# Kernel optimization log

Hardware: AMD Instinct MI355X
Metric: run time of the kernel (lower is better)

The kernel has to match this reference:

```python
import jax, jax.numpy as jnp
import numpy as np

B, S, E, H = 2, 2048, 2048, 32
D = E // H  # head_dim = 64
SCALE = D ** -0.5


def setup_inputs() -> dict:
    key = jax.random.key(0)
    ks = jax.random.split(key, 9)
    std = E ** -0.5
    return {
        "hidden_states": jax.random.normal(ks[0], (B, S, E), dtype=jnp.float32),
        "Wq": jax.random.normal(ks[1], (E, E), dtype=jnp.float32) * std,
        "bq": jax.random.normal(ks[2], (E,), dtype=jnp.float32) * 0.02,
        "Wk": jax.random.normal(ks[3], (E, E), dtype=jnp.float32) * std,
        "bk": jax.random.normal(ks[4], (E,), dtype=jnp.float32) * 0.02,
        "Wv": jax.random.normal(ks[5], (E, E), dtype=jnp.float32) * std,
        "bv": jax.random.normal(ks[6], (E,), dtype=jnp.float32) * 0.02,
        "Wo": jax.random.normal(ks[7], (E, E), dtype=jnp.float32) * std,
        "bo": jax.random.normal(ks[8], (E,), dtype=jnp.float32) * 0.02,
    }


def reference(hidden_states, Wq, bq, Wk, bk, Wv, bv, Wo, bo):
    # QKV projections (torch Linear: x @ W.T + b)
    q = hidden_states @ Wq.T + bq  # [B,S,E]
    k = hidden_states @ Wk.T + bk
    v = hidden_states @ Wv.T + bv
    # split heads -> [B,S,H,D]
    q = q.reshape(B, S, H, D)
    k = k.reshape(B, S, H, D)
    v = v.reshape(B, S, H, D)
    # causal scaled dot-product attention (prefill path of paged attention)
    scores = jnp.einsum("bqhd,bkhd->bhqk", q, k) * SCALE  # [B,H,S,S]
    causal = jnp.tril(jnp.ones((S, S), dtype=bool))
    scores = jnp.where(causal, scores, jnp.finfo(scores.dtype).min)
    probs = jax.nn.softmax(scores, axis=-1)
    attn = jnp.einsum("bhqk,bkhd->bqhd", probs, v).reshape(B, S, E)
    # output projection
    return attn @ Wo.T + bo
```

## Files before the change

kernel.cpp:

```cpp
#include <hip/hip_runtime.h>
#include <hip/hip_bf16.h>

#define B_ 2
#define S_ 2048
#define E_ 2048
#define H_ 32
#define D_ 64
#define SCALE_L2E 0.18033688f

typedef __attribute__((ext_vector_type(8))) short short8_t;
typedef __attribute__((ext_vector_type(4))) float float4_t;
typedef __attribute__((ext_vector_type(16))) float f32x16;
typedef unsigned int uint;
typedef __attribute__((ext_vector_type(4))) uint uint4_t;

__device__ __forceinline__ short f2bf(float f) {
  union { float f; unsigned u; } x; x.f = f;
  unsigned r = x.u + 0x7fffu + ((x.u >> 16) & 1u);
  return (short)(r >> 16);
}

__device__ __forceinline__ void gload_lds16(const void* g, void* l) {
  __builtin_amdgcn_global_load_lds((const __attribute__((address_space(1))) void*)g,
                                   (__attribute__((address_space(3))) void*)l, 16, 0, 0);
}

__device__ __forceinline__ uint cvt_pk_bf16(float lo, float hi) {
  uint r;
  asm volatile("v_cvt_pk_bf16_f32 %0, %1, %2" : "=v"(r) : "v"(lo), "v"(hi));
  return r;
}

__device__ __forceinline__ void pl32swap(uint& a, uint& b) {
  asm volatile("v_permlane32_swap_b32 %0, %1" : "+v"(a), "+v"(b));
}

__device__ __forceinline__ f32x16 zero16() {
  f32x16 v;
#pragma unroll
  for (int i = 0; i < 16; ++i) v[i] = 0.f;
  return v;
}

__global__ void cast_bf16_kernel(const float* __restrict__ in, short* __restrict__ out, int n4) {
  const int stride = gridDim.x * blockDim.x;
  for (int j = blockIdx.x * blockDim.x + threadIdx.x; j < n4; j += stride) {
    const float4 v = ((const float4*)in)[j];
    short4 r;
    r.x = f2bf(v.x); r.y = f2bf(v.y); r.z = f2bf(v.z); r.w = f2bf(v.w);
    ((short4*)out)[j] = r;
  }
}

__global__ void cast3_bf16(const float* __restrict__ a, const float* __restrict__ b,
                           const float* __restrict__ c, short* __restrict__ out) {
  constexpr int n4 = (E_ * E_) / 4;
  const int stride = gridDim.x * blockDim.x;
  for (int j = blockIdx.x * blockDim.x + threadIdx.x; j < 3 * n4; j += stride) {
    const float* src = (j < n4) ? a : (j < 2 * n4 ? b : c);
    const int idx = j & (n4 - 1);
    const float4 v = ((const float4*)src)[idx];
    short4 r;
    r.x = f2bf(v.x); r.y = f2bf(v.y); r.z = f2bf(v.z); r.w = f2bf(v.w);
    ((short4*)out)[j] = r;
  }
}

__global__ __launch_bounds__(512, 2) void gemm384_qkv(const short* __restrict__ A,
                                                      const short* __restrict__ Wt,
                                                      const float* __restrict__ bq,
                                                      const float* __restrict__ bk,
                                                      const float* __restrict__ bv,
                                                      short* __restrict__ Qb,
                                                      short* __restrict__ Kb,
                                                      short* __restrict__ Vb) {
  extern __shared__ __align__(16) char lds[];
  constexpr int K = E_, NT = K / 64;
  const int tid = threadIdx.x, w = tid >> 6, lane = tid & 63;
  const int wr = w >> 2, wc = w & 3;
  const int m0 = blockIdx.y * 128, n0 = blockIdx.x * 384;
  const int l15 = lane & 15, l4 = lane >> 4;

  const int sr = lane >> 2;
  const int ss = lane & 3;
  const char* aBase;
  const char* bBase[3];
  {
    const int ra = w * 16 + sr;
    aBase = (const char*)A + (size_t)(m0 + ra) * (K * 2) + ((ss ^ ((ra >> 1) & 3)) * 16);
#pragma unroll
    for (int g = 0; g < 3; ++g) {
      const int rb = g * 128 + w * 16 + sr;
      bBase[g] = (const char*)Wt + (size_t)(n0 + rb) * (K * 2) + ((ss ^ ((rb >> 1) & 3)) * 16);
    }
  }

  auto stageA = [&](int buf, int ks, int kt) {
    gload_lds16(aBase + kt * 128 + ks * 64, lds + (buf * 2 + ks) * 8192 + w * 1024);
  };
  auto stageB = [&](int buf, int ks, int kt) {
    char* base = lds + 32768 + (buf * 2 + ks) * 24576 + w * 1024;
#pragma unroll
    for (int g = 0; g < 3; ++g)
      gload_lds16(bBase[g] + kt * 128 + ks * 64, base + g * 8192);
  };
  auto ldA = [&](int buf, int ks, int i) {
    const int lr = wr * 64 + i * 16 + l15;
    return *(const short8_t*)(lds + (buf * 2 + ks) * 8192 + lr * 64 +
                              ((l4 * 16) ^ (((lr >> 1) & 3) << 4)));
  };
  auto ldB = [&](int buf, int ks, int j) {
    const int lc = wc * 96 + j * 16 + l15;
    return *(const short8_t*)(lds + 32768 + (buf * 2 + ks) * 24576 + lc * 64 +
                              ((l4 * 16) ^ (((lc >> 1) & 3) << 4)));
  };

  float4_t acc[4][6];
#pragma unroll
  for (int i = 0; i < 4; ++i)
#pragma unroll
    for (int j = 0; j < 6; ++j) acc[i][j] = (float4_t){0.f, 0.f, 0.f, 0.f};

  stageA(0, 0, 0);
  stageB(0, 0, 0);
  stageA(0, 1, 0);
  stageB(0, 1, 0);

  short8_t a_[4], b_[6];
  for (int t = 0; t < NT; ++t) {
    const int c = t & 1;
#pragma unroll
    for (int ks = 0; ks < 2; ++ks) {
      if (t + 1 < NT) {
        stageA(c ^ 1, ks, t + 1);
        stageB(c ^ 1, ks, t + 1);
        asm volatile("s_waitcnt vmcnt(8)" ::: "memory");
      } else if (ks == 0) {
        asm volatile("s_waitcnt vmcnt(4)" ::: "memory");
      } else {
        asm volatile("s_waitcnt vmcnt(0)" ::: "memory");
      }
      __builtin_amdgcn_s_barrier();
      asm volatile("" ::: "memory");
#pragma unroll
      for (int i = 0; i < 4; ++i) a_[i] = ldA(c, ks, i);
#pragma unroll
      for (int j = 0; j < 6; ++j) b_[j] = ldB(c, ks, j);
      asm volatile("s_waitcnt lgkmcnt(0)" ::: "memory");
      __builtin_amdgcn_sched_barrier(0);
      __builtin_amdgcn_s_setprio(1);
#pragma unroll
      for (int i = 0; i < 4; ++i)
#pragma unroll
        for (int j = 0; j < 6; ++j)
          acc[i][j] = __builtin_amdgcn_mfma_f32_16x16x32_bf16(a_[i], b_[j], acc[i][j], 0, 0, 0);
      __builtin_amdgcn_s_setprio(0);
    }
  }

  __syncthreads();
  const int rg = l4 * 4;
  const int b = m0 >> 11;
  const int mloc = m0 & (S_ - 1);
  char* scratch = lds + w * 2048;
#pragma unroll
  for (int j = 0; j < 6; ++j) {
    const int gc0 = n0 + wc * 96 + j * 16;
    const int seg = gc0 >> 11;
    const int ncol = gc0 & 2047;
    if (seg == 2) {
      const float bvv = bv[ncol + l15];
      asm volatile("" ::: "memory");
#pragma unroll
      for (int i = 0; i < 4; ++i) {
        short4 v;
        v.x = f2bf(acc[i][j][0] + bvv);
        v.y = f2bf(acc[i][j][1] + bvv);
        v.z = f2bf(acc[i][j][2] + bvv);
        v.w = f2bf(acc[i][j][3] + bvv);
        *(short4*)(scratch + l15 * 128 + (((i * 16 + rg) * 2) ^ ((l15 & 7) << 4))) = v;
      }
      asm volatile("s_waitcnt lgkmcnt(0)" ::: "memory");
      __builtin_amdgcn_sched_barrier(0);
#pragma unroll
      for (int half = 0; half < 2; ++half) {
        const int n = (lane >> 3) + half * 8;
        const int mb = (lane & 7) * 16;
        const short8_t vv =
            *(const short8_t*)(scratch + n * 128 + (mb ^ ((n & 7) << 4)));
        *(short8_t*)(Vb + ((size_t)(b * E_ + ncol + n)) * S_ + mloc + wr * 64 + (mb >> 1)) = vv;
      }
      asm volatile("s_waitcnt lgkmcnt(0)" ::: "memory");
      __builtin_amdgcn_sched_barrier(0);
    } else {
      const float* bias = seg ? bk : bq;
      short* Out = seg ? Kb : Qb;
      const float sc = seg ? 1.0f : SCALE_L2E;
      const int col = ncol + l15;
      const float bvv = bias[col];
#pragma unroll
      for (int i = 0; i < 4; ++i)
#pragma unroll
        for (int ii = 0; ii < 4; ++ii)
          Out[(size_t)(m0 + wr * 64 + i * 16 + rg + ii) * E_ + col] =
              f2bf((acc[i][j][ii] + bvv) * sc);
    }
  }
}

__global__ __launch_bounds__(512, 2) void gemm_o8(const short* __restrict__ A,
                                                  const short* __restrict__ Wt,
                                                  const float* __restrict__ bias,
                                                  float* __restrict__ Fout) {
  extern __shared__ __align__(16) char lds[];
  constexpr int K = E_, NT = K / 64;
  const int tid = threadIdx.x, w = tid >> 6, lane = tid & 63;
  const int wr = w >> 2, wc = w & 3;
  const int m0 = blockIdx.y * 128, n0 = blockIdx.x * 256;
  const int l15 = lane & 15, l4 = lane >> 4;

  const int sr = lane >> 2;
  const int ss = lane & 3;
  const char* aBase;
  const char* bBase0;
  const char* bBase1;
  {
    const int ra = w * 16 + sr;
    aBase = (const char*)A + (size_t)(m0 + ra) * (K * 2) + ((ss ^ ((ra >> 1) & 3)) * 16);
    const int rb0 = w * 16 + sr;
    bBase0 = (const char*)Wt + (size_t)(n0 + rb0) * (K * 2) + ((ss ^ ((rb0 >> 1) & 3)) * 16);
    const int rb1 = 128 + w * 16 + sr;
    bBase1 = (const char*)Wt + (size_t)(n0 + rb1) * (K * 2) + ((ss ^ ((rb1 >> 1) & 3)) * 16);
  }

  auto stageA = [&](int dbuf, int ks, int kt) {
    gload_lds16(aBase + kt * 128 + ks * 64, lds + (dbuf * 2 + ks) * 8192 + w * 1024);
  };
  auto stageB = [&](int dbuf, int ks, int kt) {
    char* base = lds + 32768 + (dbuf * 2 + ks) * 16384 + w * 1024;
    gload_lds16(bBase0 + kt * 128 + ks * 64, base);
    gload_lds16(bBase1 + kt * 128 + ks * 64, base + 8192);
  };
  auto ldA = [&](int dbuf, int ks, int i) {
    const int lr = wr * 64 + i * 16 + l15;
    return *(const short8_t*)(lds + (dbuf * 2 + ks) * 8192 + lr * 64 +
                              ((l4 * 16) ^ (((lr >> 1) & 3) << 4)));
  };
  auto ldB = [&](int dbuf, int ks, int j) {
    const int lc = wc * 64 + j * 16 + l15;
    return *(const short8_t*)(lds + 32768 + (dbuf * 2 + ks) * 16384 + lc * 64 +
                              ((l4 * 16) ^ (((lc >> 1) & 3) << 4)));
  };

  float4_t acc[4][4];
#pragma unroll
  for (int i = 0; i < 4; ++i)
#pragma unroll
    for (int j = 0; j < 4; ++j) acc[i][j] = (float4_t){0.f, 0.f, 0.f, 0.f};

  stageA(0, 0, 0);
  stageB(0, 0, 0);
  stageA(0, 1, 0);
  stageB(0, 1, 0);

  short8_t a_[4], b_[4];
  for (int t = 0; t < NT; ++t) {
    const int c = t & 1;
#pragma unroll
    for (int ks = 0; ks < 2; ++ks) {
      if (t + 1 < NT) {
        stageA(c ^ 1, ks, t + 1);
        stageB(c ^ 1, ks, t + 1);
        asm volatile("s_waitcnt vmcnt(6)" ::: "memory");
      } else if (ks == 0) {
        asm volatile("s_waitcnt vmcnt(3)" ::: "memory");
      } else {
        asm volatile("s_waitcnt vmcnt(0)" ::: "memory");
      }
      __builtin_amdgcn_s_barrier();
      asm volatile("" ::: "memory");
#pragma unroll
      for (int i = 0; i < 4; ++i) a_[i] = ldA(c, ks, i);
#pragma unroll
      for (int j = 0; j < 4; ++j) b_[j] = ldB(c, ks, j);
      asm volatile("s_waitcnt lgkmcnt(0)" ::: "memory");
      __builtin_amdgcn_sched_barrier(0);
      __builtin_amdgcn_s_setprio(1);
#pragma unroll
      for (int i = 0; i < 4; ++i)
#pragma unroll
        for (int j = 0; j < 4; ++j)
          acc[i][j] = __builtin_amdgcn_mfma_f32_16x16x32_bf16(a_[i], b_[j], acc[i][j], 0, 0, 0);
      __builtin_amdgcn_s_setprio(0);
    }
  }

  const int rg = l4 * 4;
#pragma unroll
  for (int j = 0; j < 4; ++j) {
    const int col = n0 + wc * 64 + j * 16 + l15;
    const float bvv = bias[col];
#pragma unroll
    for (int i = 0; i < 4; ++i)
#pragma unroll
      for (int ii = 0; ii < 4; ++ii)
        Fout[(size_t)(m0 + wr * 64 + i * 16 + rg + ii) * E_ + col] = acc[i][j][ii] + bvv;
  }
}

__global__ __launch_bounds__(512, 2) void attn_fwd(const short* __restrict__ Qg,
                                                   const short* __restrict__ Kg,
                                                   const short* __restrict__ Vt,
                                                   short* __restrict__ Og) {
  __shared__ __align__(16) short lds[16384];
  const int tid = threadIdx.x, w = tid >> 6, lane = tid & 63;
  const int l31 = lane & 31, hh = lane >> 5;
  const int bh = blockIdx.x;
  const int b = bh >> 5, h = bh & 31;
  const int pq = blockIdx.y;

  const char* Kgb = (const char*)(Kg + (size_t)b * S_ * E_ + h * D_);
  const char* Vgb = (const char*)(Vt + (size_t)bh * 64 * S_);

  const int srow = w * 8 + (lane >> 3);
  const int sb = (lane & 7) * 16;
  const int ssw = (srow & 7) << 4;

#pragma unroll 1
  for (int ph = 0; ph < 2; ++ph) {
    const int qt = ph ? (7 - pq) : pq;
    const int q0 = qt * 256;
    const int qwmin = q0 + w * 32;
    const int qg = qwmin + l31;

    const short* qr = Qg + ((size_t)(b * S_ + qg)) * E_ + h * D_;
    short8_t qf[4];
#pragma unroll
    for (int dblk = 0; dblk < 4; ++dblk)
      qf[dblk] = *(const short8_t*)(qr + dblk * 16 + hh * 8);

    f32x16 o0 = zero16(), o1 = zero16();
    float m_run = -1e30f, l_run = 0.f;

    const int nt = 4 * qt + 4;
    const int ntw = (qwmin + 31) / 64 + 1;

    gload_lds16(Kgb + (size_t)srow * 4096 + (sb ^ ssw), lds + w * 512);
    gload_lds16(Vgb + (size_t)srow * 4096 + (sb ^ ssw), lds + 4096 + w * 512);
    __syncthreads();

    int cur = 0;
    for (int t = 0; t < nt; ++t) {
      if (t + 1 < nt) {
        const int k0n = (t + 1) * 64;
        short* kb = lds + (cur ^ 1) * 8192 + w * 512;
        gload_lds16(Kgb + (size_t)(k0n + srow) * 4096 + (sb ^ ssw), kb);
        gload_lds16(Vgb + (size_t)srow * 4096 + (size_t)k0n * 2 + (sb ^ ssw), kb + 4096);
      }

      if (t < ntw) {
        const int k0 = t * 64;
        const char* Kc = (const char*)lds + cur * 16384;
        const char* Vc = Kc + 8192;
        const int xs = (l31 & 7) << 4;

        f32x16 st0 = zero16(), st1 = zero16();
#pragma unroll
        for (int dblk = 0; dblk < 4; ++dblk) {
          const int off = (dblk * 32 + hh * 16) ^ xs;
          const short8_t kf0 = *(const short8_t*)(Kc + l31 * 128 + off);
          const short8_t kf1 = *(const short8_t*)(Kc + (32 + l31) * 128 + off);
          st0 = __builtin_amdgcn_mfma_f32_32x32x16_bf16(kf0, qf[dblk], st0, 0, 0, 0);
          st1 = __builtin_amdgcn_mfma_f32_32x32x16_bf16(kf1, qf[dblk], st1, 0, 0, 0);
        }

        if (k0 + 63 > qwmin) {
#pragma unroll
          for (int r = 0; r < 16; ++r) {
            const int kvr = k0 + ((r & 3) + 8 * (r >> 2) + 4 * hh);
            if (kvr > qg) st0[r] = -1e30f;
            if (kvr + 32 > qg) st1[r] = -1e30f;
          }
        }

        float mv = -1e30f;
#pragma unroll
        for (int r = 0; r < 16; ++r) mv = fmaxf(mv, fmaxf(st0[r], st1[r]));
        mv = fmaxf(mv, __shfl_xor(mv, 32));
        const float mnew = fmaxf(m_run, mv);
        const float alpha = exp2f(m_run - mnew);
        m_run = mnew;
        float sum = 0.f;
#pragma unroll
        for (int r = 0; r < 16; ++r) {
          st0[r] = exp2f(st0[r] - mnew);
          st1[r] = exp2f(st1[r] - mnew);
          sum += st0[r] + st1[r];
        }
        sum += __shfl_xor(sum, 32);
        l_run = l_run * alpha + sum;
        o0 = o0 * alpha;
        o1 = o1 * alpha;

        uint pk_[16];
#pragma unroll
        for (int j = 0; j < 8; ++j) pk_[j] = cvt_pk_bf16(st0[2 * j], st0[2 * j + 1]);
#pragma unroll
        for (int j = 0; j < 8; ++j) pk_[8 + j] = cvt_pk_bf16(st1[2 * j], st1[2 * j + 1]);
        pl32swap(pk_[0], pk_[2]);  pl32swap(pk_[1], pk_[3]);
        pl32swap(pk_[4], pk_[6]);  pl32swap(pk_[5], pk_[7]);
        pl32swap(pk_[8], pk_[10]); pl32swap(pk_[9], pk_[11]);
        pl32swap(pk_[12], pk_[14]); pl32swap(pk_[13], pk_[15]);
        uint4_t paw[4];
#pragma unroll
        for (int f = 0; f < 4; ++f)
          paw[f] = (uint4_t){pk_[4 * f], pk_[4 * f + 1], pk_[4 * f + 2], pk_[4 * f + 3]};

#pragma unroll
        for (int kb = 0; kb < 4; ++kb) {
          const short8_t pa = *(const short8_t*)&paw[kb];
          const int off = (kb * 32 + hh * 16) ^ xs;
          const short8_t vf0 = *(const short8_t*)(Vc + l31 * 128 + off);
          const short8_t vf1 = *(const short8_t*)(Vc + (32 + l31) * 128 + off);
          o0 = __builtin_amdgcn_mfma_f32_32x32x16_bf16(vf0, pa, o0, 0, 0, 0);
          o1 = __builtin_amdgcn_mfma_f32_32x32x16_bf16(vf1, pa, o1, 0, 0, 0);
        }
      }

      __syncthreads();
      cur ^= 1;
    }

    {
      short* ow = lds + w * 2048;
      const float inv = 1.0f / l_run;
#pragma unroll
      for (int r = 0; r < 16; ++r) {
        const int d = (r & 3) + 8 * (r >> 2) + 4 * hh;
        const int x = (l31 & 7) << 4;
        *(short*)((char*)ow + l31 * 128 + ((d * 2) ^ x)) = f2bf(o0[r] * inv);
        *(short*)((char*)ow + l31 * 128 + (((d + 32) * 2) ^ x)) = f2bf(o1[r] * inv);
      }
#pragma unroll
      for (int pz = 0; pz < 4; ++pz) {
        const int qloc = pz * 8 + (lane >> 3);
        const int sbyte = (lane & 7) * 16;
        const short8_t vv = *(const short8_t*)((char*)ow + qloc * 128 + (sbyte ^ ((qloc & 7) << 4)));
        *(short8_t*)(Og + ((size_t)(b * S_ + q0 + w * 32 + qloc)) * E_ + h * 64 + (lane & 7) * 8) = vv;
      }
    }
    __syncthreads();
  }
}

extern "C" void kernel_launch(void* const* d_in, const int* in_sizes, int n_in,
                              void* d_out, int out_size, void* d_ws, size_t ws_size,
                              hipStream_t stream) {
  const float* X  = (const float*)d_in[0];
  const float* Wq = (const float*)d_in[1];
  const float* bq = (const float*)d_in[2];
  const float* Wk = (const float*)d_in[3];
  const float* bk = (const float*)d_in[4];
  const float* Wv = (const float*)d_in[5];
  const float* bv = (const float*)d_in[6];
  const float* Wo = (const float*)d_in[7];
  const float* bo = (const float*)d_in[8];

  const size_t NX = (size_t)B_ * S_ * E_;
  const size_t NW = (size_t)E_ * E_;

  short* ws = (short*)d_ws;
  short* Xb = ws;
  short* Wb = Xb + NX;
  short* Kb = Wb + 3 * NW;
  short* Vb = Kb + NX;
  short* Qb = (short*)d_out;
  short* Ab = Xb;

  (void)hipFuncSetAttribute((const void*)gemm384_qkv,
                            hipFuncAttributeMaxDynamicSharedMemorySize, 131072);
  (void)hipFuncSetAttribute((const void*)gemm_o8,
                            hipFuncAttributeMaxDynamicSharedMemorySize, 98304);

  cast_bf16_kernel<<<2048, 256, 0, stream>>>(X, Xb, (int)(NX / 4));
  cast3_bf16<<<3072, 256, 0, stream>>>(Wq, Wk, Wv, Wb);

  gemm384_qkv<<<dim3(16, 32), 512, 131072, stream>>>(Xb, Wb, bq, bk, bv, Qb, Kb, Vb);

  cast_bf16_kernel<<<1024, 256, 0, stream>>>(Wo, Wb, (int)(NW / 4));

  attn_fwd<<<dim3(B_ * H_, 4), 512, 0, stream>>>(Qb, Kb, Vb, Ab);

  gemm_o8<<<dim3(E_ / 256, B_ * S_ / 128), 512, 98304, stream>>>(Ab, Wb, bo, (float*)d_out);
}
```

Before: 251.2 us.

## Split QKV GEMM into 256x256 Q/K GEMM and separate V GEMM, fuse casts

Replaces the single 128x384-tile QKV projection with a 256x256-tile kernel for Q and K and a separate 128x256-tile kernel for V, which keeps the transposed epilogue. The X and Wq/Wk/Wv casts are merged into one launch. The larger Q/K tile raises arithmetic intensity per LDS byte and removes per-column segment branching in the epilogue. The cost is an extra GEMM launch and a smaller V grid that may leave the GPU underfilled, plus higher register use from the 8x4 accumulators.

```diff
diff --git a/kernel.cpp b/kernel.cpp
--- a/kernel.cpp
+++ b/kernel.cpp
@@ -40,6 +40,29 @@
 #pragma unroll
   for (int i = 0; i < 16; ++i) v[i] = 0.f;
   return v;
+}
+
+__global__ void cast_xw(const float* __restrict__ X, const float* __restrict__ Wq,
+                        const float* __restrict__ Wk, const float* __restrict__ Wv,
+                        short* __restrict__ out) {
+  constexpr int nX = 1 << 21, nW = 1 << 20, total = nX + 3 * nW;
+  const int stride = gridDim.x * blockDim.x;
+  for (int j = blockIdx.x * blockDim.x + threadIdx.x; j < total; j += stride) {
+    const float* src;
+    int idx;
+    if (j < nX) {
+      src = X; idx = j;
+    } else {
+      const int jw = j - nX;
+      const int sel = jw >> 20;
+      idx = jw & (nW - 1);
+      src = sel == 0 ? Wq : (sel == 1 ? Wk : Wv);
+    }
+    const float4 v = ((const float4*)src)[idx];
+    short4 r;
+    r.x = f2bf(v.x); r.y = f2bf(v.y); r.z = f2bf(v.z); r.w = f2bf(v.w);
+    ((short4*)out)[j] = r;
+  }
 }
 
 __global__ void cast_bf16_kernel(const float* __restrict__ in, short* __restrict__ out, int n4) {
@@ -52,81 +75,64 @@
   }
 }
 
-__global__ void cast3_bf16(const float* __restrict__ a, const float* __restrict__ b,
-                           const float* __restrict__ c, short* __restrict__ out) {
-  constexpr int n4 = (E_ * E_) / 4;
-  const int stride = gridDim.x * blockDim.x;
-  for (int j = blockIdx.x * blockDim.x + threadIdx.x; j < 3 * n4; j += stride) {
-    const float* src = (j < n4) ? a : (j < 2 * n4 ? b : c);
-    const int idx = j & (n4 - 1);
-    const float4 v = ((const float4*)src)[idx];
-    short4 r;
-    r.x = f2bf(v.x); r.y = f2bf(v.y); r.z = f2bf(v.z); r.w = f2bf(v.w);
-    ((short4*)out)[j] = r;
-  }
-}
-
-__global__ __launch_bounds__(512, 2) void gemm384_qkv(const short* __restrict__ A,
-                                                      const short* __restrict__ Wt,
-                                                      const float* __restrict__ bq,
-                                                      const float* __restrict__ bk,
-                                                      const float* __restrict__ bv,
-                                                      short* __restrict__ Qb,
-                                                      short* __restrict__ Kb,
-                                                      short* __restrict__ Vb) {
+__global__ __launch_bounds__(512, 2) void gemm256_qk(const short* __restrict__ A,
+                                                     const short* __restrict__ Wt,
+                                                     const float* __restrict__ bq,
+                                                     const float* __restrict__ bk,
+                                                     short* __restrict__ Qb,
+                                                     short* __restrict__ Kb) {
   extern __shared__ __align__(16) char lds[];
   constexpr int K = E_, NT = K / 64;
   const int tid = threadIdx.x, w = tid >> 6, lane = tid & 63;
   const int wr = w >> 2, wc = w & 3;
-  const int m0 = blockIdx.y * 128, n0 = blockIdx.x * 384;
+  const int m0 = blockIdx.y * 256, n0 = blockIdx.x * 256;
   const int l15 = lane & 15, l4 = lane >> 4;
 
   const int sr = lane >> 2;
   const int ss = lane & 3;
-  const char* aBase;
-  const char* bBase[3];
-  {
-    const int ra = w * 16 + sr;
-    aBase = (const char*)A + (size_t)(m0 + ra) * (K * 2) + ((ss ^ ((ra >> 1) & 3)) * 16);
-#pragma unroll
-    for (int g = 0; g < 3; ++g) {
-      const int rb = g * 128 + w * 16 + sr;
-      bBase[g] = (const char*)Wt + (size_t)(n0 + rb) * (K * 2) + ((ss ^ ((rb >> 1) & 3)) * 16);
-    }
+  const char* aB[2];
+  const char* bB[2];
+#pragma unroll
+  for (int g = 0; g < 2; ++g) {
+    const int r = w * 32 + g * 16 + sr;
+    aB[g] = (const char*)A + (size_t)(m0 + r) * (K * 2) + ((ss ^ ((r >> 1) & 3)) * 16);
+    bB[g] = (const char*)Wt + (size_t)(n0 + r) * (K * 2) + ((ss ^ ((r >> 1) & 3)) * 16);
   }
 
   auto stageA = [&](int buf, int ks, int kt) {
-    gload_lds16(aBase + kt * 128 + ks * 64, lds + (buf * 2 + ks) * 8192 + w * 1024);
+#pragma unroll
+    for (int g = 0; g < 2; ++g)
+      gload_lds16(aB[g] + kt * 128 + ks * 64, lds + (buf * 2 + ks) * 16384 + w * 2048 + g * 1024);
   };
   auto stageB = [&](int buf, int ks, int kt) {
-    char* base = lds + 32768 + (buf * 2 + ks) * 24576 + w * 1024;
-#pragma unroll
-    for (int g = 0; g < 3; ++g)
-      gload_lds16(bBase[g] + kt * 128 + ks * 64, base + g * 8192);
+#pragma unroll
+    for (int g = 0; g < 2; ++g)
+      gload_lds16(bB[g] + kt * 128 + ks * 64,
+                  lds + 65536 + (buf * 2 + ks) * 16384 + w * 2048 + g * 1024);
   };
   auto ldA = [&](int buf, int ks, int i) {
-    const int lr = wr * 64 + i * 16 + l15;
-    return *(const short8_t*)(lds + (buf * 2 + ks) * 8192 + lr * 64 +
+    const int lr = wr * 128 + i * 16 + l15;
+    return *(const short8_t*)(lds + (buf * 2 + ks) * 16384 + lr * 64 +
                               ((l4 * 16) ^ (((lr >> 1) & 3) << 4)));
   };
   auto ldB = [&](int buf, int ks, int j) {
-    const int lc = wc * 96 + j * 16 + l15;
-    return *(const short8_t*)(lds + 32768 + (buf * 2 + ks) * 24576 + lc * 64 +
+    const int lc = wc * 64 + j * 16 + l15;
+    return *(const short8_t*)(lds + 65536 + (buf * 2 + ks) * 16384 + lc * 64 +
                               ((l4 * 16) ^ (((lc >> 1) & 3) << 4)));
   };
 
-  float4_t acc[4][6];
-#pragma unroll
-  for (int i = 0; i < 4; ++i)
-#pragma unroll
-    for (int j = 0; j < 6; ++j) acc[i][j] = (float4_t){0.f, 0.f, 0.f, 0.f};
+  float4_t acc[8][4];
+#pragma unroll
+  for (int i = 0; i < 8; ++i)
+#pragma unroll
+    for (int j = 0; j < 4; ++j) acc[i][j] = (float4_t){0.f, 0.f, 0.f, 0.f};
 
   stageA(0, 0, 0);
   stageB(0, 0, 0);
   stageA(0, 1, 0);
   stageB(0, 1, 0);
 
-  short8_t a_[4], b_[6];
+  short8_t a_[8], b_[4];
   for (int t = 0; t < NT; ++t) {
     const int c = t & 1;
 #pragma unroll
@@ -143,75 +149,44 @@
       __builtin_amdgcn_s_barrier();
       asm volatile("" ::: "memory");
 #pragma unroll
-      for (int i = 0; i < 4; ++i) a_[i] = ldA(c, ks, i);
-#pragma unroll
-      for (int j = 0; j < 6; ++j) b_[j] = ldB(c, ks, j);
+      for (int i = 0; i < 8; ++i) a_[i] = ldA(c, ks, i);
+#pragma unroll
+      for (int j = 0; j < 4; ++j) b_[j] = ldB(c, ks, j);
       asm volatile("s_waitcnt lgkmcnt(0)" ::: "memory");
       __builtin_amdgcn_sched_barrier(0);
       __builtin_amdgcn_s_setprio(1);
 #pragma unroll
-      for (int i = 0; i < 4; ++i)
-#pragma unroll
-        for (int j = 0; j < 6; ++j)
+      for (int i = 0; i < 8; ++i)
+#pragma unroll
+        for (int j = 0; j < 4; ++j)
           acc[i][j] = __builtin_amdgcn_mfma_f32_16x16x32_bf16(a_[i], b_[j], acc[i][j], 0, 0, 0);
       __builtin_amdgcn_s_setprio(0);
     }
   }
 
-  __syncthreads();
+  const int seg = n0 >> 11;
+  const int ncol = n0 & 2047;
+  const float* bias = seg ? bk : bq;
+  short* Out = seg ? Kb : Qb;
+  const float sc = seg ? 1.0f : SCALE_L2E;
   const int rg = l4 * 4;
-  const int b = m0 >> 11;
-  const int mloc = m0 & (S_ - 1);
-  char* scratch = lds + w * 2048;
-#pragma unroll
-  for (int j = 0; j < 6; ++j) {
-    const int gc0 = n0 + wc * 96 + j * 16;
-    const int seg = gc0 >> 11;
-    const int ncol = gc0 & 2047;
-    if (seg == 2) {
-      const float bvv = bv[ncol + l15];
-      asm volatile("" ::: "memory");
-#pragma unroll
-      for (int i = 0; i < 4; ++i) {
-        short4 v;
-        v.x = f2bf(acc[i][j][0] + bvv);
-        v.y = f2bf(acc[i][j][1] + bvv);
-        v.z = f2bf(acc[i][j][2] + bvv);
-        v.w = f2bf(acc[i][j][3] + bvv);
-        *(short4*)(scratch + l15 * 128 + (((i * 16 + rg) * 2) ^ ((l15 & 7) << 4))) = v;
-      }
-      asm volatile("s_waitcnt lgkmcnt(0)" ::: "memory");
-      __builtin_amdgcn_sched_barrier(0);
-#pragma unroll
-      for (int half = 0; half < 2; ++half) {
-        const int n = (lane >> 3) + half * 8;
-        const int mb = (lane & 7) * 16;
-        const short8_t vv =
-            *(const short8_t*)(scratch + n * 128 + (mb ^ ((n & 7) << 4)));
-        *(short8_t*)(Vb + ((size_t)(b * E_ + ncol + n)) * S_ + mloc + wr * 64 + (mb >> 1)) = vv;
-      }
-      asm volatile("s_waitcnt lgkmcnt(0)" ::: "memory");
-      __builtin_amdgcn_sched_barrier(0);
-    } else {
-      const float* bias = seg ? bk : bq;
-      short* Out = seg ? Kb : Qb;
-      const float sc = seg ? 1.0f : SCALE_L2E;
-      const int col = ncol + l15;
-      const float bvv = bias[col];
-#pragma unroll
-      for (int i = 0; i < 4; ++i)
-#pragma unroll
-        for (int ii = 0; ii < 4; ++ii)
-          Out[(size_t)(m0 + wr * 64 + i * 16 + rg + ii) * E_ + col] =
-              f2bf((acc[i][j][ii] + bvv) * sc);
-    }
-  }
-}
-
-__global__ __launch_bounds__(512, 2) void gemm_o8(const short* __restrict__ A,
-                                                  const short* __restrict__ Wt,
-                                                  const float* __restrict__ bias,
-                                                  float* __restrict__ Fout) {
+#pragma unroll
+  for (int j = 0; j < 4; ++j) {
+    const int col = ncol + wc * 64 + j * 16 + l15;
+    const float bvv = bias[col];
+#pragma unroll
+    for (int i = 0; i < 8; ++i)
+#pragma unroll
+      for (int ii = 0; ii < 4; ++ii)
+        Out[(size_t)(m0 + wr * 128 + i * 16 + rg + ii) * E_ + col] =
+            f2bf((acc[i][j][ii] + bvv) * sc);
+  }
+}
+
+__global__ __launch_bounds__(512, 2) void gemm_v128(const short* __restrict__ A,
+                                                    const short* __restrict__ Wt,
+                                                    const float* __restrict__ bv,
+                                                    short* __restrict__ Vb) {
   extern __shared__ __align__(16) char lds[];
   constexpr int K = E_, NT = K / 64;
   const int tid = threadIdx.x, w = tid >> 6, lane = tid & 63;
@@ -295,6 +270,126 @@
     }
   }
 
+  __syncthreads();
+  const int rg = l4 * 4;
+  const int b = m0 >> 11;
+  const int mloc = m0 & (S_ - 1);
+  char* scratch = lds + w * 2048;
+#pragma unroll
+  for (int j = 0; j < 4; ++j) {
+    const int ncol = n0 + wc * 64 + j * 16;
+    const float bvv = bv[ncol + l15];
+    asm volatile("" ::: "memory");
+#pragma unroll
+    for (int i = 0; i < 4; ++i) {
+      short4 v;
+      v.x = f2bf(acc[i][j][0] + bvv);
+      v.y = f2bf(acc[i][j][1] + bvv);
+      v.z = f2bf(acc[i][j][2] + bvv);
+      v.w = f2bf(acc[i][j][3] + bvv);
+      *(short4*)(scratch + l15 * 128 + (((i * 16 + rg) * 2) ^ ((l15 & 7) << 4))) = v;
+    }
+    asm volatile("s_waitcnt lgkmcnt(0)" ::: "memory");
+    __builtin_amdgcn_sched_barrier(0);
+#pragma unroll
+    for (int half = 0; half < 2; ++half) {
+      const int n = (lane >> 3) + half * 8;
+      const int mb = (lane & 7) * 16;
+      const short8_t vv = *(const short8_t*)(scratch + n * 128 + (mb ^ ((n & 7) << 4)));
+      *(short8_t*)(Vb + ((size_t)(b * E_ + ncol + n)) * S_ + mloc + wr * 64 + (mb >> 1)) = vv;
+    }
+    asm volatile("s_waitcnt lgkmcnt(0)" ::: "memory");
+    __builtin_amdgcn_sched_barrier(0);
+  }
+}
+
+__global__ __launch_bounds__(512, 2) void gemm_o8(const short* __restrict__ A,
+                                                  const short* __restrict__ Wt,
+                                                  const float* __restrict__ bias,
+                                                  float* __restrict__ Fout) {
+  extern __shared__ __align__(16) char lds[];
+  constexpr int K = E_, NT = K / 64;
+  const int tid = threadIdx.x, w = tid >> 6, lane = tid & 63;
+  const int wr = w >> 2, wc = w & 3;
+  const int m0 = blockIdx.y * 128, n0 = blockIdx.x * 256;
+  const int l15 = lane & 15, l4 = lane >> 4;
+
+  const int sr = lane >> 2;
+  const int ss = lane & 3;
+  const char* aBase;
+  const char* bBase0;
+  const char* bBase1;
+  {
+    const int ra = w * 16 + sr;
+    aBase = (const char*)A + (size_t)(m0 + ra) * (K * 2) + ((ss ^ ((ra >> 1) & 3)) * 16);
+    const int rb0 = w * 16 + sr;
+    bBase0 = (const char*)Wt + (size_t)(n0 + rb0) * (K * 2) + ((ss ^ ((rb0 >> 1) & 3)) * 16);
+    const int rb1 = 128 + w * 16 + sr;
+    bBase1 = (const char*)Wt + (size_t)(n0 + rb1) * (K * 2) + ((ss ^ ((rb1 >> 1) & 3)) * 16);
+  }
+
+  auto stageA = [&](int dbuf, int ks, int kt) {
+    gload_lds16(aBase + kt * 128 + ks * 64, lds + (dbuf * 2 + ks) * 8192 + w * 1024);
+  };
+  auto stageB = [&](int dbuf, int ks, int kt) {
+    char* base = lds + 32768 + (dbuf * 2 + ks) * 16384 + w * 1024;
+    gload_lds16(bBase0 + kt * 128 + ks * 64, base);
+    gload_lds16(bBase1 + kt * 128 + ks * 64, base + 8192);
+  };
+  auto ldA = [&](int dbuf, int ks, int i) {
+    const int lr = wr * 64 + i * 16 + l15;
+    return *(const short8_t*)(lds + (dbuf * 2 + ks) * 8192 + lr * 64 +
+                              ((l4 * 16) ^ (((lr >> 1) & 3) << 4)));
+  };
+  auto ldB = [&](int dbuf, int ks, int j) {
+    const int lc = wc * 64 + j * 16 + l15;
+    return *(const short8_t*)(lds + 32768 + (dbuf * 2 + ks) * 16384 + lc * 64 +
+                              ((l4 * 16) ^ (((lc >> 1) & 3) << 4)));
+  };
+
+  float4_t acc[4][4];
+#pragma unroll
+  for (int i = 0; i < 4; ++i)
+#pragma unroll
+    for (int j = 0; j < 4; ++j) acc[i][j] = (float4_t){0.f, 0.f, 0.f, 0.f};
+
+  stageA(0, 0, 0);
+  stageB(0, 0, 0);
+  stageA(0, 1, 0);
+  stageB(0, 1, 0);
+
+  short8_t a_[4], b_[4];
+  for (int t = 0; t < NT; ++t) {
+    const int c = t & 1;
+#pragma unroll
+    for (int ks = 0; ks < 2; ++ks) {
+      if (t + 1 < NT) {
+        stageA(c ^ 1, ks, t + 1);
+        stageB(c ^ 1, ks, t + 1);
+        asm volatile("s_waitcnt vmcnt(6)" ::: "memory");
+      } else if (ks == 0) {
+        asm volatile("s_waitcnt vmcnt(3)" ::: "memory");
+      } else {
+        asm volatile("s_waitcnt vmcnt(0)" ::: "memory");
+      }
+      __builtin_amdgcn_s_barrier();
+      asm volatile("" ::: "memory");
+#pragma unroll
+      for (int i = 0; i < 4; ++i) a_[i] = ldA(c, ks, i);
+#pragma unroll
+      for (int j = 0; j < 4; ++j) b_[j] = ldB(c, ks, j);
+      asm volatile("s_waitcnt lgkmcnt(0)" ::: "memory");
+      __builtin_amdgcn_sched_barrier(0);
+      __builtin_amdgcn_s_setprio(1);
+#pragma unroll
+      for (int i = 0; i < 4; ++i)
+#pragma unroll
+        for (int j = 0; j < 4; ++j)
+          acc[i][j] = __builtin_amdgcn_mfma_f32_16x16x32_bf16(a_[i], b_[j], acc[i][j], 0, 0, 0);
+      __builtin_amdgcn_s_setprio(0);
+    }
+  }
+
   const int rg = l4 * 4;
 #pragma unroll
   for (int j = 0; j < 4; ++j) {
@@ -477,15 +572,17 @@
   short* Qb = (short*)d_out;
   short* Ab = Xb;
 
-  (void)hipFuncSetAttribute((const void*)gemm384_qkv,
+  (void)hipFuncSetAttribute((const void*)gemm256_qk,
                             hipFuncAttributeMaxDynamicSharedMemorySize, 131072);
+  (void)hipFuncSetAttribute((const void*)gemm_v128,
+                            hipFuncAttributeMaxDynamicSharedMemorySize, 98304);
   (void)hipFuncSetAttribute((const void*)gemm_o8,
                             hipFuncAttributeMaxDynamicSharedMemorySize, 98304);
 
-  cast_bf16_kernel<<<2048, 256, 0, stream>>>(X, Xb, (int)(NX / 4));
-  cast3_bf16<<<3072, 256, 0, stream>>>(Wq, Wk, Wv, Wb);
-
-  gemm384_qkv<<<dim3(16, 32), 512, 131072, stream>>>(Xb, Wb, bq, bk, bv, Qb, Kb, Vb);
+  cast_xw<<<2048, 256, 0, stream>>>(X, Wq, Wk, Wv, Xb);
+
+  gemm256_qk<<<dim3(16, 16), 512, 131072, stream>>>(Xb, Wb, bq, bk, Qb, Kb);
+  gemm_v128<<<dim3(8, 32), 512, 98304, stream>>>(Xb, Wb + 2 * NW, bv, Vb);
 
   cast_bf16_kernel<<<1024, 256, 0, stream>>>(Wo, Wb, (int)(NW / 4));
 
```

Result: slower. 258.9 us (+3.1%).
